# Kernel optimization log

Measured on AMD Instinct MI355X. Metric: run time of the kernel, lower is better.

The kernel has to match this reference:

```python
import jax, jax.numpy as jnp
import numpy as np

NL_IN = 0.5      # init kwarg nl_in
CONS = 1e-10     # epsilon added to rates
POISSON_GAIN = 20.0

def setup_inputs() -> dict:
    key = jax.random.key(0)
    k1, k2 = jax.random.split(key)
    shape = (8, 4, 28, 256, 256)  # (bs, c, s, h, w)
    spec_data = jax.random.uniform(k1, shape, dtype=jnp.float32)
    filt = jax.random.uniform(k2, shape, dtype=jnp.float32)
    return {"spec_data": spec_data, "filter": filt}

def reference(spec_data, filter):
    # cap_data = sum over (channel, spectral) dims -> [bs, h, w], then [bs, h, w, 1]
    cap = jnp.sum(spec_data * filter, axis=(1, 2))[..., None]

    # noise synthesis (need_noise=True path)
    poisson_t = jnp.full_like(cap, POISSON_GAIN * NL_IN)
    dark_t = jnp.full_like(cap, 1.0 * NL_IN)
    gauss_t = jnp.full_like(cap, 1.0 * NL_IN)
    peak = cap + CONS

    key = jax.random.key(1)
    kp, kd, kg = jax.random.split(key, 3)
    pnoisy = jax.random.poisson(kp, peak).astype(cap.dtype)
    dnoisy = jax.random.poisson(kd, dark_t).astype(cap.dtype)
    gnoisy = jax.random.normal(kg, cap.shape, dtype=cap.dtype) * gauss_t

    noisy = (pnoisy + dnoisy + gnoisy) * poisson_t / 255.0
    return (noisy, peak, dark_t, gauss_t ** 2)
```

## Files before the change

### kernel.cpp

```cpp
#include <hip/hip_runtime.h>
#include <cstdint>
#include <cstddef>

#pragma clang fp contract(off)

#define N_PIX    524288
#define CSPLANES 112
#define PLANE    65536
#define DCH      48

struct TF2 { uint32_t a, b; };

__host__ __device__ constexpr uint32_t rotl32(uint32_t x, int d) {
  return (x << d) | (x >> (32 - d));
}

__host__ __device__ constexpr TF2 threefry(uint32_t k0, uint32_t k1,
                                           uint32_t c0, uint32_t c1) {
  uint32_t ks2 = k0 ^ k1 ^ 0x1BD11BDAu;
  uint32_t x0 = c0 + k0;
  uint32_t x1 = c1 + k1;
  const int R0[4] = {13, 15, 26, 6};
  const int R1[4] = {17, 29, 16, 24};
  for (int i = 0; i < 4; ++i) { x0 += x1; x1 = rotl32(x1, R0[i]); x1 ^= x0; }
  x0 += k1;  x1 += ks2 + 1u;
  for (int i = 0; i < 4; ++i) { x0 += x1; x1 = rotl32(x1, R1[i]); x1 ^= x0; }
  x0 += ks2; x1 += k0 + 2u;
  for (int i = 0; i < 4; ++i) { x0 += x1; x1 = rotl32(x1, R0[i]); x1 ^= x0; }
  x0 += k0;  x1 += k1 + 3u;
  for (int i = 0; i < 4; ++i) { x0 += x1; x1 = rotl32(x1, R1[i]); x1 ^= x0; }
  x0 += k1;  x1 += ks2 + 4u;
  for (int i = 0; i < 4; ++i) { x0 += x1; x1 = rotl32(x1, R0[i]); x1 ^= x0; }
  x0 += ks2; x1 += k0 + 5u;
  return TF2{x0, x1};
}

struct Chains {
  uint32_t kg0, kg1;
  uint32_t rj0a[DCH], rj0b[DCH], rj1a[DCH], rj1b[DCH];
  uint32_t kda[DCH], kdb[DCH];
  uint32_t kpa[DCH], kpb[DCH];
};

__host__ __device__ constexpr Chains make_chains() {
  Chains c{};
  TF2 kp = threefry(0u, 1u, 0u, 0u);
  TF2 kd = threefry(0u, 1u, 0u, 1u);
  TF2 kg = threefry(0u, 1u, 0u, 2u);
  c.kg0 = kg.a; c.kg1 = kg.b;
  {
    uint32_t a = kp.a, b = kp.b;
    for (int i = 0; i < DCH; ++i) {
      TF2 nk = threefry(a, b, 0u, 0u);
      TF2 s0 = threefry(a, b, 0u, 1u);
      TF2 s1 = threefry(a, b, 0u, 2u);
      c.rj0a[i] = s0.a; c.rj0b[i] = s0.b;
      c.rj1a[i] = s1.a; c.rj1b[i] = s1.b;
      a = nk.a; b = nk.b;
    }
  }
  {
    uint32_t a = kd.a, b = kd.b;
    for (int i = 0; i < DCH; ++i) {
      TF2 nk = threefry(a, b, 0u, 0u);
      TF2 sk = threefry(a, b, 0u, 1u);
      c.kda[i] = sk.a; c.kdb[i] = sk.b;
      a = nk.a; b = nk.b;
    }
  }
  {
    uint32_t a = kp.a, b = kp.b;
    for (int i = 0; i < DCH; ++i) {
      TF2 nk = threefry(a, b, 0u, 0u);
      TF2 sk = threefry(a, b, 0u, 1u);
      c.kpa[i] = sk.a; c.kpb[i] = sk.b;
      a = nk.a; b = nk.b;
    }
  }
  return c;
}

__constant__ Chains G = make_chains();

__device__ inline float u01(uint32_t k0, uint32_t k1, uint32_t j) {
  TF2 r = threefry(k0, k1, 0u, j);
  uint32_t bits = r.a ^ r.b;
  return __uint_as_float((bits >> 9) | 0x3F800000u) - 1.0f;
}

__device__ inline float xla_lgamma(float x_in) {
  float z = x_in - 1.0f;
  float x = 1.0f;
  x = x + 676.520368121885098567009190444019f    / ((z + 0.0f) + 1.0f);
  x = x + (-1259.13921672240287047156078755283f) / ((z + 1.0f) + 1.0f);
  x = x + 771.3234287776530788486528258894f      / ((z + 2.0f) + 1.0f);
  x = x + (-176.61502916214059906584551354f)     / ((z + 3.0f) + 1.0f);
  x = x + 12.507343278686904814458936853f        / ((z + 4.0f) + 1.0f);
  x = x + (-0.13857109526572011689554707f)       / ((z + 5.0f) + 1.0f);
  x = x + 9.984369578019570859563e-6f            / ((z + 6.0f) + 1.0f);
  x = x + 1.50563273514931155834e-7f             / ((z + 7.0f) + 1.0f);
  float t = 7.5f + z;
  float log_t = 2.0149030205422647f + log1pf(z / 7.5f);
  return 0.91893853320467274178f + ((z + 0.5f) - t / log_t) * log_t + logf(x);
}

__device__ inline float xla_erfinv(float xx) {
  float w = -log1pf(-(xx * xx));
  float p;
  if (w < 5.0f) {
    float ww = w - 2.5f;
    p = 2.81022636e-08f;
    p = 3.43273939e-07f + p * ww;
    p = -3.5233877e-06f + p * ww;
    p = -4.39150654e-06f + p * ww;
    p = 0.00021858087f + p * ww;
    p = -0.00125372503f + p * ww;
    p = -0.00417768164f + p * ww;
    p = 0.246640727f + p * ww;
    p = 1.50140941f + p * ww;
  } else {
    float ww = sqrtf(w) - 3.0f;
    p = -0.000200214257f;
    p = 0.000100950558f + p * ww;
    p = 0.00134934322f + p * ww;
    p = -0.00367342844f + p * ww;
    p = 0.00573950773f + p * ww;
    p = -0.0076224613f + p * ww;
    p = 0.00943887047f + p * ww;
    p = 1.00167406f + p * ww;
    p = 2.83297682f + p * ww;
  }
  return p * xx;
}

__device__ inline float xla_normal(uint32_t j) {
  const float lo = -0.999999940395355224609375f;
  float f = u01(G.kg0, G.kg1, j);
  float u = f * (1.0f - lo) + lo;
  u = fmaxf(lo, u);
  return 1.41421356237309504880f * xla_erfinv(u);
}

__device__ inline int knuth_sample(const uint32_t* ka, const uint32_t* kb,
                                   uint32_t j, float lam) {
  const float neg = -lam;
  int k = 0;
  float lp = 0.0f;
  #pragma unroll 1
  for (int i = 0; i < DCH; ++i) {
    if (!(lp > neg)) break;
    ++k;
    float uu = u01(ka[i], kb[i], j);
    lp = lp + logf(uu);
  }
  return k - 1;
}

struct RejC { float lam, loglam, a, b, inva, vr; };

__device__ inline RejC make_rc(float lam) {
  RejC rc;
  rc.lam = lam;
  rc.loglam = logf(lam);
  rc.b = 0.931f + 2.53f * sqrtf(lam);
  rc.a = -0.059f + 0.02483f * rc.b;
  rc.inva = 1.1239f + 1.1328f / (rc.b - 3.4f);
  rc.vr = 0.9277f - 3.6224f / (rc.b - 2.0f);
  return rc;
}

__device__ inline bool rej_step(const RejC& rc, uint32_t j, int i, float* kout) {
  float u = u01(G.rj0a[i], G.rj0b[i], j) - 0.5f;
  float v = u01(G.rj1a[i], G.rj1b[i], j);
  float us = 0.5f - fabsf(u);
  float k = floorf(((2.0f * rc.a / us + rc.b) * u + rc.lam) + 0.43f);
  *kout = k;
  bool accept1 = (us >= 0.07f) && (v <= rc.vr);
  if (accept1) return true;
  bool reject = (k < 0.0f) || ((us < 0.013f) && (v > us));
  if (reject) return false;
  float s = logf(v * rc.inva / (rc.a / (us * us) + rc.b));
  float t = (-rc.lam + k * rc.loglam) - xla_lgamma(k + 1.0f);
  return s <= t;
}

__device__ __noinline__ void process_pixel(uint32_t j, float cap,
                                           float& pk, float& dn, float& gn,
                                           unsigned& F) {
  float peak = cap + 1e-10f;
  pk = peak;
  dn = (float)knuth_sample(G.kda, G.kdb, j, 0.5f);
  gn = xla_normal(j) * 0.5f;
  RejC rc = make_rc(peak);
  unsigned f = DCH;
  #pragma unroll 1
  for (int i = 0; i < DCH; ++i) {
    float kc;
    if (rej_step(rc, j, i, &kc)) { f = (unsigned)(i + 1); break; }
  }
  F = f;
}

__global__ __launch_bounds__(128) void cap_kernel(const float* __restrict__ spec,
                                                  const float* __restrict__ filt,
                                                  float* __restrict__ out,
                                                  unsigned* __restrict__ tslot) {
  const int tid = blockIdx.x * 128 + threadIdx.x;
  const int p = tid << 2;
  const int b = p >> 16;
  const int hw = p & 65535;
  const float* sp = spec + (size_t)b * ((size_t)CSPLANES * PLANE) + hw;
  const float* fp = filt + (size_t)b * ((size_t)CSPLANES * PLANE) + hw;
  float ax = 0.f, ay = 0.f, az = 0.f, aw = 0.f;
  #pragma unroll 4
  for (int cs = 0; cs < CSPLANES; ++cs) {
    const float4 s = *reinterpret_cast<const float4*>(sp + (size_t)cs * PLANE);
    const float4 f = *reinterpret_cast<const float4*>(fp + (size_t)cs * PLANE);
    ax += s.x * f.x; ay += s.y * f.y; az += s.z * f.z; aw += s.w * f.w;
  }

  float4 pk4, dn4, gn4;
  unsigned F0, F1, F2, F3;
  process_pixel((uint32_t)p + 0u, ax, pk4.x, dn4.x, gn4.x, F0);
  process_pixel((uint32_t)p + 1u, ay, pk4.y, dn4.y, gn4.y, F1);
  process_pixel((uint32_t)p + 2u, az, pk4.z, dn4.z, gn4.z, F2);
  process_pixel((uint32_t)p + 3u, aw, pk4.w, dn4.w, gn4.w, F3);

  reinterpret_cast<float4*>(out + N_PIX)[tid] = pk4;
  reinterpret_cast<float4*>(out)[tid] = dn4;
  reinterpret_cast<float4*>(out + 2 * N_PIX)[tid] = gn4;

  unsigned Fm0 = F0 > F1 ? F0 : F1;
  unsigned Fm1 = F2 > F3 ? F2 : F3;
  unsigned Fm = Fm0 > Fm1 ? Fm0 : Fm1;
  for (int off = 32; off; off >>= 1) {
    unsigned o = (unsigned)__shfl_down((int)Fm, off, 64);
    Fm = Fm > o ? Fm : o;
  }
  __shared__ unsigned sred[2];
  if ((threadIdx.x & 63) == 0) sred[threadIdx.x >> 6] = Fm;
  __syncthreads();
  if (threadIdx.x == 0) {
    unsigned m = sred[0] > sred[1] ? sred[0] : sred[1];
    atomicMax(tslot, m);
  }
}

__global__ __launch_bounds__(256) void resolve_kernel(float* __restrict__ out,
                                                      const unsigned* __restrict__ tslot) {
  const uint32_t j = blockIdx.x * 256u + threadIdx.x;
  const int T = (int)(*tslot);
  const float peak = out[N_PIX + j];
  const float d = out[j];
  const float g = out[2 * N_PIX + j];
  float pv;
  if (peak >= 10.0f) {
    RejC rc = make_rc(peak);
    float kk = -1.0f;
    #pragma unroll 1
    for (int i = T - 1; i >= 0; --i) {
      float kc;
      if (rej_step(rc, j, i, &kc)) { kk = kc; break; }
    }
    pv = (float)(int)kk;
  } else if (peak <= 0.0f) {
    pv = 0.0f;
  } else {
    pv = (float)knuth_sample(G.kpa, G.kpb, j, peak);
  }
  const float noisy = ((pv + d) + g) * 10.0f / 255.0f;
  out[j] = noisy;
  out[2 * N_PIX + j] = 0.5f;
  out[3 * N_PIX + j] = 0.25f;
}

extern "C" void kernel_launch(void* const* d_in, const int* in_sizes, int n_in,
                              void* d_out, int out_size, void* d_ws, size_t ws_size,
                              hipStream_t stream) {
  (void)in_sizes; (void)n_in; (void)out_size; (void)ws_size;
  const float* spec = (const float*)d_in[0];
  const float* filt = (const float*)d_in[1];
  float* out = (float*)d_out;
  unsigned* tslot = (unsigned*)d_ws;
  (void)hipMemsetAsync(d_ws, 0, sizeof(unsigned), stream);
  hipLaunchKernelGGL(cap_kernel, dim3(1024), dim3(128), 0, stream,
                     spec, filt, out, tslot);
  hipLaunchKernelGGL(resolve_kernel, dim3(2048), dim3(256), 0, stream,
                     out, tslot);
}
```

Baseline: 504.9 us.

## Split channel reduction across warps into separate kernel from noise synthesis

Separates the spectral-filter reduction into its own kernel where four wavefronts each reduce a quarter of the channel-spectral planes and combine via shared memory. This gives many more threads in flight for the bandwidth-bound stream. RNG noise generation and the rejection-count max move to a per-pixel noise kernel. This adds one launch and an extra round trip of the cap buffer through global memory, and changes the floating-point summation order.

```diff
diff --git a/kernel.cpp b/kernel.cpp
--- a/kernel.cpp
+++ b/kernel.cpp
@@ -184,64 +184,69 @@
   return s <= t;
 }
 
-__device__ __noinline__ void process_pixel(uint32_t j, float cap,
-                                           float& pk, float& dn, float& gn,
-                                           unsigned& F) {
-  float peak = cap + 1e-10f;
-  pk = peak;
-  dn = (float)knuth_sample(G.kda, G.kdb, j, 0.5f);
-  gn = xla_normal(j) * 0.5f;
+__global__ __launch_bounds__(256, 8) void reduce_kernel(const float* __restrict__ spec,
+                                                        const float* __restrict__ filt,
+                                                        float* __restrict__ out) {
+  const int tid = threadIdx.x;
+  const int w = tid >> 6;
+  const int l = tid & 63;
+  const int pixbase = blockIdx.x << 8;
+  const int b_img = pixbase >> 16;
+  const int hw = (pixbase & 65535) + (l << 2);
+  const size_t base = (size_t)b_img * ((size_t)CSPLANES * PLANE)
+                    + (size_t)(w * 28) * PLANE + (size_t)hw;
+  const float* sp = spec + base;
+  const float* fp = filt + base;
+
+  float ax = 0.f, ay = 0.f, az = 0.f, aw = 0.f;
+  #pragma unroll 4
+  for (int cs = 0; cs < 28; ++cs) {
+    const float4 s = *reinterpret_cast<const float4*>(sp + (size_t)cs * PLANE);
+    const float4 f = *reinterpret_cast<const float4*>(fp + (size_t)cs * PLANE);
+    ax += s.x * f.x; ay += s.y * f.y; az += s.z * f.z; aw += s.w * f.w;
+  }
+
+  __shared__ float part[4][64][4];
+  part[w][l][0] = ax; part[w][l][1] = ay; part[w][l][2] = az; part[w][l][3] = aw;
+  __syncthreads();
+
+  const int g = tid >> 2, c = tid & 3;
+  float c0 = part[0][g][c];
+  float c1 = part[1][g][c];
+  float c2 = part[2][g][c];
+  float c3 = part[3][g][c];
+  float cap = ((c0 + c1) + c2) + c3;
+  out[N_PIX + pixbase + tid] = cap;
+}
+
+__global__ __launch_bounds__(256) void noise_kernel(float* __restrict__ out,
+                                                    unsigned* __restrict__ tslot) {
+  const uint32_t j = blockIdx.x * 256u + threadIdx.x;
+  const float cap = out[N_PIX + j];
+  const float peak = cap + 1e-10f;
+  out[N_PIX + j] = peak;
+  out[j] = (float)knuth_sample(G.kda, G.kdb, j, 0.5f);
+  out[2 * N_PIX + j] = xla_normal(j) * 0.5f;
+
   RejC rc = make_rc(peak);
-  unsigned f = DCH;
+  unsigned F = DCH;
   #pragma unroll 1
   for (int i = 0; i < DCH; ++i) {
     float kc;
-    if (rej_step(rc, j, i, &kc)) { f = (unsigned)(i + 1); break; }
-  }
-  F = f;
-}
-
-__global__ __launch_bounds__(128) void cap_kernel(const float* __restrict__ spec,
-                                                  const float* __restrict__ filt,
-                                                  float* __restrict__ out,
-                                                  unsigned* __restrict__ tslot) {
-  const int tid = blockIdx.x * 128 + threadIdx.x;
-  const int p = tid << 2;
-  const int b = p >> 16;
-  const int hw = p & 65535;
-  const float* sp = spec + (size_t)b * ((size_t)CSPLANES * PLANE) + hw;
-  const float* fp = filt + (size_t)b * ((size_t)CSPLANES * PLANE) + hw;
-  float ax = 0.f, ay = 0.f, az = 0.f, aw = 0.f;
-  #pragma unroll 4
-  for (int cs = 0; cs < CSPLANES; ++cs) {
-    const float4 s = *reinterpret_cast<const float4*>(sp + (size_t)cs * PLANE);
-    const float4 f = *reinterpret_cast<const float4*>(fp + (size_t)cs * PLANE);
-    ax += s.x * f.x; ay += s.y * f.y; az += s.z * f.z; aw += s.w * f.w;
-  }
-
-  float4 pk4, dn4, gn4;
-  unsigned F0, F1, F2, F3;
-  process_pixel((uint32_t)p + 0u, ax, pk4.x, dn4.x, gn4.x, F0);
-  process_pixel((uint32_t)p + 1u, ay, pk4.y, dn4.y, gn4.y, F1);
-  process_pixel((uint32_t)p + 2u, az, pk4.z, dn4.z, gn4.z, F2);
-  process_pixel((uint32_t)p + 3u, aw, pk4.w, dn4.w, gn4.w, F3);
-
-  reinterpret_cast<float4*>(out + N_PIX)[tid] = pk4;
-  reinterpret_cast<float4*>(out)[tid] = dn4;
-  reinterpret_cast<float4*>(out + 2 * N_PIX)[tid] = gn4;
-
-  unsigned Fm0 = F0 > F1 ? F0 : F1;
-  unsigned Fm1 = F2 > F3 ? F2 : F3;
-  unsigned Fm = Fm0 > Fm1 ? Fm0 : Fm1;
+    if (rej_step(rc, j, i, &kc)) { F = (unsigned)(i + 1); break; }
+  }
+
   for (int off = 32; off; off >>= 1) {
-    unsigned o = (unsigned)__shfl_down((int)Fm, off, 64);
-    Fm = Fm > o ? Fm : o;
-  }
-  __shared__ unsigned sred[2];
-  if ((threadIdx.x & 63) == 0) sred[threadIdx.x >> 6] = Fm;
+    unsigned o = (unsigned)__shfl_down((int)F, off, 64);
+    F = F > o ? F : o;
+  }
+  __shared__ unsigned sred[4];
+  if ((threadIdx.x & 63) == 0) sred[threadIdx.x >> 6] = F;
   __syncthreads();
   if (threadIdx.x == 0) {
-    unsigned m = sred[0] > sred[1] ? sred[0] : sred[1];
+    unsigned m0 = sred[0] > sred[1] ? sred[0] : sred[1];
+    unsigned m1 = sred[2] > sred[3] ? sred[2] : sred[3];
+    unsigned m = m0 > m1 ? m0 : m1;
     atomicMax(tslot, m);
   }
 }
@@ -283,8 +288,10 @@
   float* out = (float*)d_out;
   unsigned* tslot = (unsigned*)d_ws;
   (void)hipMemsetAsync(d_ws, 0, sizeof(unsigned), stream);
-  hipLaunchKernelGGL(cap_kernel, dim3(1024), dim3(128), 0, stream,
-                     spec, filt, out, tslot);
-  hipLaunchKernelGGL(resolve_kernel, dim3(2048), dim3(256), 0, stream,
+  hipLaunchKernelGGL(reduce_kernel, dim3(N_PIX / 256), dim3(256), 0, stream,
+                     spec, filt, out);
+  hipLaunchKernelGGL(noise_kernel, dim3(N_PIX / 256), dim3(256), 0, stream,
                      out, tslot);
-}
+  hipLaunchKernelGGL(resolve_kernel, dim3(N_PIX / 256), dim3(256), 0, stream,
+                     out, tslot);
+}
```

After: 505.7 us. Within noise of the previous version (+0.2%).
